# Performance work log

Hardware: AMD Instinct MI355X
Metric: run time of the kernel (lower is better)

Reference implementation:

```python
import jax, jax.numpy as jnp
import numpy as np

NEG = -1e18


def _split_heads(x, h):
    # [B, L, D] -> [B, H, L, D/H]
    b, l, d = x.shape
    return x.reshape(b, l, h, d // h).transpose(0, 2, 1, 3)


def _merge_heads(x):
    # [B, H, L, Dh] -> [B, L, H*Dh]
    b, h, l, dh = x.shape
    return x.transpose(0, 2, 1, 3).reshape(b, l, h * dh)


def _sparse(att, dp_map):
    # att: [B, H, L] per-token scores; dp_map: [B, 2, L] (row, col) tree indices.
    # scatter att[b,h,t] -> S[b, h, dp_map[b,0,t], dp_map[b,1,t]], then symmetrize.
    B, H, L = att.shape
    bi = jnp.arange(B)[:, None, None]          # [B,1,1]
    hi = jnp.arange(H)[None, :, None]          # [1,H,1]
    p0 = dp_map[:, 0, :][:, None, :]           # [B,1,L]
    p1 = dp_map[:, 1, :][:, None, :]           # [B,1,L]
    s = jnp.zeros((B, H, L, L), att.dtype)
    s = s.at[bi, hi, p0, p1].set(att)          # matches torch index_put_ (overwrite)
    return s + jnp.swapaxes(s, 2, 3)


def _reverse(values, dp_map):
    # r[b, j] = values[b, dp_map[b,0,j]] for j >= 1; r[b,0] = 0
    idx = dp_map[:, 0, :]                      # [B, L]
    r = jnp.take_along_axis(values, idx[:, :, None], axis=1)
    return r.at[:, 0, :].set(0.0)


def setup_inputs() -> dict:
    key = jax.random.key(0)
    ks = jax.random.split(key, 16)
    B, L, D, R, H = 16, 384, 768, 768, 12
    inp = {
        "queries":   jax.random.normal(ks[0], (B, L, D), jnp.float32),
        "keys":      jax.random.normal(ks[1], (B, L, D), jnp.float32),
        "values":    jax.random.normal(ks[2], (B, L, D), jnp.float32),
        "relations": jax.random.normal(ks[3], (B, L, R), jnp.float32),
        "dp_map":    jax.random.randint(ks[4], (B, 2, L), 0, L, jnp.int32),
        "mask":      jax.random.bernoulli(ks[5], 0.1, (B, L, L)),
        "rel_mask":  jax.random.bernoulli(ks[6], 0.1, (B, L, 1)),
        "Wq":  jax.random.normal(ks[7],  (D, D), jnp.float32) * 0.02,
        "Wk":  jax.random.normal(ks[8],  (D, D), jnp.float32) * 0.02,
        "Wv":  jax.random.normal(ks[9],  (D, D), jnp.float32) * 0.02,
        "Wo":  jax.random.normal(ks[10], (D, D), jnp.float32) * 0.02,
        "Wge": jax.random.normal(ks[11], (D, R), jnp.float32) * 0.02,
        "Wgr": jax.random.normal(ks[12], (R, R), jnp.float32) * 0.02,
        "Vr":  jax.random.normal(ks[13], (R, 1), jnp.float32) * 0.02,
        "Vg":  jax.random.normal(ks[14], (R, 1), jnp.float32) * 0.02,
    }
    return inp


def reference(queries, keys, values, relations, dp_map, mask, rel_mask,
              Wq, Wk, Wv, Wo, Wge, Wgr, Vr, Vg):
    H = 12
    R = Vg.shape[0]
    Dk = Wq.shape[1]
    scale = (Dk // H) ** -0.5

    # config.is_reverse = True path
    hv = jnp.where(rel_mask, 0.0, _reverse(values, dp_map))       # [B,L,D]
    rel = jnp.where(rel_mask, 0.0, relations)                     # [B,L,R]

    # semantic gated mechanism
    rv_h = _split_heads(rel @ Wgr, H)                             # [B,H,L,R/H]
    hs_h = _split_heads(hv @ Wge, H)
    Vg_h = Vg.reshape(H, R // H, 1)
    g = jnp.tanh(jnp.einsum('bhld,hdo->bhlo', hs_h + rv_h, Vg_h))[..., 0]
    gated = _sparse(g, dp_map)                                    # [B,H,L,L]

    q = _split_heads(queries @ Wq, H) * scale
    k = _split_heads(keys @ Wk, H)
    v = _split_heads(values @ Wv, H)
    rel_h = _split_heads(rel, H)
    Vr_h = Vr.reshape(H, R // H, 1)

    self_logits = jnp.einsum('bhqd,bhkd->bhqk', q, k)             # [B,H,L,L]
    rel_logits = _sparse(jnp.einsum('bhld,hdo->bhlo', rel_h, Vr_h)[..., 0], dp_map)

    m = mask[:, None]                                             # [B,1,L,L]
    self_logits = jnp.where(m, NEG, self_logits)
    rel_logits = jnp.where(m, NEG, rel_logits)

    attention_weights = self_logits.sum(axis=1) / H               # [B,L,L]
    sw = jax.nn.softmax(self_logits, axis=-1)
    rw = jax.nn.softmax(rel_logits, axis=-1)
    w = (1.0 - gated) * sw + gated * rw                           # dropout p=0

    ctx = jnp.einsum('bhqk,bhkd->bhqd', w, v)
    out = _merge_heads(ctx) @ Wo
    return out, attention_weights
```

## Files before the change

### kernel.cpp

```cpp
#include <hip/hip_runtime.h>
#include <math.h>

#define Bn 16
#define Lq 384
#define Hn 12
#define Dm 768
#define DH 64
#define QT2 16
#define NEGV (-1e18f)
#define SPAD 402

typedef __attribute__((ext_vector_type(4))) float f32x4;
typedef __attribute__((ext_vector_type(8))) __bf16 bf16x8;
typedef __attribute__((ext_vector_type(4))) __bf16 bf16x4;
typedef unsigned short ushort_t;
typedef unsigned int uint_t;

__device__ __forceinline__ ushort_t f2b(float f) {
  unsigned int u = __float_as_uint(f);
  unsigned int r = (u + 0x7FFFu + ((u >> 16) & 1u)) >> 16;
  return (ushort_t)r;
}
__device__ __forceinline__ bf16x8 cvt8(float4 a, float4 b) {
  bf16x8 r;
  r[0] = (__bf16)a.x; r[1] = (__bf16)a.y; r[2] = (__bf16)a.z; r[3] = (__bf16)a.w;
  r[4] = (__bf16)b.x; r[5] = (__bf16)b.y; r[6] = (__bf16)b.z; r[7] = (__bf16)b.w;
  return r;
}

__global__ __launch_bounds__(256) void k_prep_age(
    const float* __restrict__ Wge, const float* __restrict__ Wgr,
    const float* __restrict__ Vg, float* __restrict__ Age, float* __restrict__ Agr)
{
  int which = blockIdx.x / Hn;
  int h = blockIdx.x % Hn;
  const float* Wsrc = which ? Wgr : Wge;
  float* dst = which ? Agr : Age;
  __shared__ float vg[DH];
  if (threadIdx.x < DH) vg[threadIdx.x] = Vg[h*DH + threadIdx.x];
  __syncthreads();
  for (int d = threadIdx.x; d < Dm; d += 256) {
    const float* wrow = Wsrc + (size_t)d*Dm + h*DH;
    float s = 0.f;
    #pragma unroll 8
    for (int j = 0; j < DH; ++j) s = fmaf(wrow[j], vg[j], s);
    dst[h*Dm + d] = s;
  }
}

__global__ void k_win(const int* __restrict__ dp, int* __restrict__ win) {
  int i = blockIdx.x*256 + threadIdx.x;
  if (i >= Bn*Lq) return;
  int b = i / Lq, l = i % Lq;
  int p0 = dp[(size_t)(b*2+0)*Lq + l];
  int p1 = dp[(size_t)(b*2+1)*Lq + l];
  atomicMax(&win[(size_t)b*Lq*Lq + (size_t)p0*Lq + p1], l);
}

__global__ __launch_bounds__(256) void k_pair(
    const int* __restrict__ win, const int* __restrict__ mask,
    uint_t* __restrict__ wpair)
{
  __shared__ int tB[32][33];
  int b = blockIdx.z;
  int i0 = blockIdx.x*32, j0 = blockIdx.y*32;
  const int* wb = win + (size_t)b*Lq*Lq;
  const int* mb = mask + (size_t)b*Lq*Lq;
  int tx = threadIdx.x & 31, ty = threadIdx.x >> 5;
  #pragma unroll
  for (int rr = 0; rr < 4; ++rr) {
    int r = ty + rr*8;
    tB[r][tx] = wb[(size_t)(j0+r)*Lq + i0 + tx];
  }
  __syncthreads();
  #pragma unroll
  for (int rr = 0; rr < 4; ++rr) {
    int ti = ty + rr*8;
    int i = i0 + ti, j = j0 + tx;
    int l1 = wb[(size_t)i*Lq + j];
    int l2 = tB[tx][ti];
    int mk = mb[(size_t)i*Lq + j];
    wpair[(size_t)b*Lq*Lq + (size_t)i*Lq + j] =
        ((uint_t)(mk != 0) << 31) | ((unsigned)(l1 + 1) << 16) | (unsigned)(l2 + 1);
  }
}

__global__ __launch_bounds__(256) void k_grlog(
    const float* __restrict__ values, const float* __restrict__ relations,
    const int* __restrict__ dp, const int* __restrict__ rel_mask,
    const float* __restrict__ Age, const float* __restrict__ Agr,
    const float* __restrict__ Vr,
    float* __restrict__ g, float* __restrict__ rlog)
{
  int blk = blockIdx.x;
  int b = blk / (Lq/4), l0 = (blk % (Lq/4))*4;
  int tid = threadIdx.x, lane = tid & 63, wave = tid >> 6;
  __shared__ float relrow[4][Dm], hvrow[4][Dm];
  #pragma unroll
  for (int rr = 0; rr < 4; ++rr) {
    int l = l0 + rr;
    int rm = rel_mask[(size_t)b*Lq + l];
    int idx = dp[(size_t)(b*2)*Lq + l];
    const float* vrow = values + ((size_t)b*Lq + idx)*Dm;
    const float* rrow = relations + ((size_t)b*Lq + l)*Dm;
    for (int d = tid; d < Dm; d += 256) {
      relrow[rr][d] = rm ? 0.f : rrow[d];
      hvrow[rr][d]  = (rm || l == 0) ? 0.f : vrow[d];
    }
  }
  __syncthreads();
  int l = l0 + wave;
  for (int h = 0; h < Hn; ++h) {
    float p = 0.f;
    #pragma unroll
    for (int k = 0; k < Dm/64; ++k) {
      int d = lane + 64*k;
      p = fmaf(hvrow[wave][d], Age[h*Dm + d],
          fmaf(relrow[wave][d], Agr[h*Dm + d], p));
    }
    #pragma unroll
    for (int o = 32; o > 0; o >>= 1) p += __shfl_xor(p, o);
    if (lane == 0) g[((size_t)b*Hn + h)*Lq + l] = tanhf(p);
  }
  if (lane < Hn) {
    float s = 0.f;
    #pragma unroll 8
    for (int j = 0; j < DH; ++j)
      s = fmaf(relrow[wave][lane*DH + j], Vr[lane*DH + j], s);
    rlog[((size_t)b*Hn + lane)*Lq + l] = s;
  }
}

__global__ __launch_bounds__(256) void k_wT4(
    const float* __restrict__ W0, const float* __restrict__ W1,
    const float* __restrict__ W2, const float* __restrict__ W3,
    ushort_t* __restrict__ T0, ushort_t* __restrict__ T1,
    ushort_t* __restrict__ T2, ushort_t* __restrict__ T3)
{
  int z = blockIdx.z;
  const float* W = (z == 0) ? W0 : (z == 1) ? W1 : (z == 2) ? W2 : W3;
  ushort_t* WT = (z == 0) ? T0 : (z == 1) ? T1 : (z == 2) ? T2 : T3;
  __shared__ float t[32][33];
  int k0 = blockIdx.x*32, n0 = blockIdx.y*32;
  int tx = threadIdx.x & 31, ty = threadIdx.x >> 5;
  #pragma unroll
  for (int r = 0; r < 4; ++r)
    t[ty + r*8][tx] = W[(size_t)(k0 + ty + r*8)*Dm + n0 + tx];
  __syncthreads();
  #pragma unroll
  for (int r = 0; r < 4; ++r)
    WT[(size_t)(n0 + ty + r*8)*Dm + k0 + tx] = f2b(t[tx][ty + r*8]);
}

__global__ __launch_bounds__(256) void k_mmqkv(
    const float* __restrict__ Xq, const float* __restrict__ Xk,
    const float* __restrict__ Xv,
    const ushort_t* __restrict__ WqT, const ushort_t* __restrict__ WkT,
    const ushort_t* __restrict__ WvT,
    ushort_t* __restrict__ qbf, ushort_t* __restrict__ kbf,
    ushort_t* __restrict__ vTbf)
{
  const int K = Dm;
  __shared__ ushort_t As[128*64];
  __shared__ ushort_t Bs[128*64];

  int z = blockIdx.z;
  const float* A     = (z == 0) ? Xq : (z == 1) ? Xk : Xv;
  const ushort_t* BT = (z == 0) ? WqT : (z == 1) ? WkT : WvT;

  int bm = blockIdx.x;
  int bn = blockIdx.y;
  int m_blk = bm*128;

  int t = threadIdx.x;
  int wave = t >> 6, lane = t & 63;
  int wr = wave >> 1, wc = wave & 1;
  int lrow = lane & 15, lkg = lane >> 4;

  f32x4 acc[4][4];
  #pragma unroll
  for (int i = 0; i < 4; ++i)
    #pragma unroll
    for (int j = 0; j < 4; ++j) acc[i][j] = (f32x4)(0.f);

  int sr = t >> 3, sc8 = t & 7;
  for (int k0 = 0; k0 < K; k0 += 64) {
    __syncthreads();
    #pragma unroll
    for (int i = 0; i < 4; ++i) {
      int row = sr + i*32;
      const float* ap = A + (size_t)(m_blk + row)*K + k0 + sc8*8;
      float4 f0 = *(const float4*)ap;
      float4 f1 = *(const float4*)(ap + 4);
      uint4 vb = *(const uint4*)(BT + (size_t)(bn*128 + row)*K + k0 + sc8*8);
      int slot = sc8 ^ (row & 7);
      *(bf16x8*)&As[row*64 + slot*8] = cvt8(f0, f1);
      *(uint4*)&Bs[row*64 + slot*8] = vb;
    }
    __syncthreads();
    #pragma unroll
    for (int kk = 0; kk < 2; ++kk) {
      bf16x8 aF[4], bF[4];
      int chunk = kk*4 + lkg;
      #pragma unroll
      for (int mi = 0; mi < 4; ++mi) {
        int arow = wr*64 + mi*16 + lrow;
        aF[mi] = *(const bf16x8*)&As[arow*64 + ((chunk ^ (arow & 7)) << 3)];
        int brow = wc*64 + mi*16 + lrow;
        bF[mi] = *(const bf16x8*)&Bs[brow*64 + ((chunk ^ (brow & 7)) << 3)];
      }
      #pragma unroll
      for (int mi = 0; mi < 4; ++mi)
        #pragma unroll
        for (int ni = 0; ni < 4; ++ni)
          acc[mi][ni] = __builtin_amdgcn_mfma_f32_16x16x32_bf16(
              aF[mi], bF[ni], acc[mi][ni], 0, 0, 0);
    }
  }

  float alpha = (z == 0) ? 0.125f : 1.f;
  #pragma unroll
  for (int mi = 0; mi < 4; ++mi) {
    #pragma unroll
    for (int ni = 0; ni < 4; ++ni) {
      f32x4 a = acc[mi][ni];
      int rit = wr*64 + mi*16 + 4*lkg;
      int cit = wc*64 + ni*16 + lrow;
      int gcol = bn*128 + cit;
      if (z < 2) {
        ushort_t* Cb = z ? kbf : qbf;
        int grow = m_blk + rit;
        #pragma unroll
        for (int r = 0; r < 4; ++r)
          Cb[(size_t)(grow + r)*Dm + gcol] = f2b(a[r]*alpha);
      } else {
        int b = bm/3;
        int rl = (bm%3)*128 + rit;
        ushort4 u;
        u.x = f2b(a[0]); u.y = f2b(a[1]); u.z = f2b(a[2]); u.w = f2b(a[3]);
        *(ushort4*)&vTbf[((size_t)b*Dm + gcol)*Lq + rl] = u;
      }
    }
  }
}

template<int MODE>
__global__ __launch_bounds__(256) void k_mm64(
    const ushort_t* __restrict__ A, const ushort_t* __restrict__ BT,
    float* __restrict__ Cf, const int* __restrict__ mask, float alpha)
{
  const int K = Dm;
  __shared__ ushort_t As[64*64];
  __shared__ ushort_t Bs[128*64];

  int bm = blockIdx.x, bn = blockIdx.y, b = blockIdx.z;
  const ushort_t* Ab = (MODE == 3) ? A  + (size_t)b*Lq*Dm : A;
  const ushort_t* Bb = (MODE == 3) ? BT + (size_t)b*Lq*Dm : BT;
  int m0 = bm*64, n0 = bn*128;

  int t = threadIdx.x;
  int wave = t >> 6, lane = t & 63;
  int wr = wave >> 1, wc = wave & 1;
  int lrow = lane & 15, lkg = lane >> 4;

  f32x4 acc[2][4];
  #pragma unroll
  for (int i = 0; i < 2; ++i)
    #pragma unroll
    for (int j = 0; j < 4; ++j) acc[i][j] = (f32x4)(0.f);

  int sr = t >> 3, sc8 = t & 7;
  for (int k0 = 0; k0 < K; k0 += 64) {
    __syncthreads();
    #pragma unroll
    for (int i = 0; i < 2; ++i) {
      int row = sr + i*32;
      uint4 va = *(const uint4*)(Ab + (size_t)(m0 + row)*K + k0 + sc8*8);
      int slot = sc8 ^ (row & 7);
      *(uint4*)&As[row*64 + slot*8] = va;
    }
    #pragma unroll
    for (int i = 0; i < 4; ++i) {
      int row = sr + i*32;
      uint4 vb = *(const uint4*)(Bb + (size_t)(n0 + row)*K + k0 + sc8*8);
      int slot = sc8 ^ (row & 7);
      *(uint4*)&Bs[row*64 + slot*8] = vb;
    }
    __syncthreads();
    #pragma unroll
    for (int kk = 0; kk < 2; ++kk) {
      bf16x8 aF[2], bF[4];
      int chunk = kk*4 + lkg;
      #pragma unroll
      for (int mi = 0; mi < 2; ++mi) {
        int arow = wr*32 + mi*16 + lrow;
        aF[mi] = *(const bf16x8*)&As[arow*64 + ((chunk ^ (arow & 7)) << 3)];
      }
      #pragma unroll
      for (int ni = 0; ni < 4; ++ni) {
        int brow = wc*64 + ni*16 + lrow;
        bF[ni] = *(const bf16x8*)&Bs[brow*64 + ((chunk ^ (brow & 7)) << 3)];
      }
      #pragma unroll
      for (int mi = 0; mi < 2; ++mi)
        #pragma unroll
        for (int ni = 0; ni < 4; ++ni)
          acc[mi][ni] = __builtin_amdgcn_mfma_f32_16x16x32_bf16(
              aF[mi], bF[ni], acc[mi][ni], 0, 0, 0);
    }
  }

  #pragma unroll
  for (int mi = 0; mi < 2; ++mi) {
    #pragma unroll
    for (int ni = 0; ni < 4; ++ni) {
      f32x4 a = acc[mi][ni];
      int rit = wr*32 + mi*16 + 4*lkg;
      int cit = wc*64 + ni*16 + lrow;
      if (MODE == 0) {
        int grow = m0 + rit, gcol = n0 + cit;
        #pragma unroll
        for (int r = 0; r < 4; ++r)
          Cf[(size_t)(grow + r)*Dm + gcol] = a[r]*alpha;
      } else {
        int rl = m0 + rit, cl = n0 + cit;
        const int* mb2 = mask + (size_t)b*Lq*Lq;
        float* awb = Cf + (size_t)b*Lq*Lq;
        #pragma unroll
        for (int r = 0; r < 4; ++r) {
          int m = mb2[(size_t)(rl + r)*Lq + cl];
          awb[(size_t)(rl + r)*Lq + cl] = m ? NEGV : a[r]*alpha;
        }
      }
    }
  }
}

__global__ __launch_bounds__(256, 5) void k_attn3(
    const ushort_t* __restrict__ qbf, const ushort_t* __restrict__ kbf,
    const ushort_t* __restrict__ vT, const uint_t* __restrict__ wpair,
    const float* __restrict__ g, const float* __restrict__ rlog,
    ushort_t* __restrict__ ctxbf)
{
  __shared__ float S[QT2][SPAD];
  __shared__ float2 rg2[Lq + 1];

  int bid = blockIdx.x;
  int h  = bid % Hn;
  int qt = (bid / Hn) % (Lq/QT2);
  int b  = bid / (Hn * (Lq/QT2));
  int q0 = qt * QT2;
  int tid = threadIdx.x, lane = tid & 63, wave = tid >> 6;
  int lrow = lane & 15, lkg = lane >> 4;
  int w4 = wave*4;

  const uint_t* wpb = wpair + (size_t)b*Lq*Lq;
  const float* gh = g    + ((size_t)b*Hn + h)*Lq;
  const float* rh = rlog + ((size_t)b*Hn + h)*Lq;

  uint_t wpre[4][6];
  #pragma unroll
  for (int r = 0; r < 4; ++r) {
    const uint_t* wrow = wpb + (size_t)(q0 + w4 + r)*Lq + lane;
    #pragma unroll
    for (int u = 0; u < 6; ++u) wpre[r][u] = wrow[u*64];
  }

  if (tid == 0) { rg2[0].x = 0.f; rg2[0].y = 0.f; }
  for (int e = tid; e < Lq; e += 256) {
    float2 v2; v2.x = rh[e]; v2.y = gh[e];
    rg2[e + 1] = v2;
  }

  {
    const ushort_t* qb = qbf + ((size_t)b*Lq + q0 + lrow)*Dm + h*DH + lkg*8;
    bf16x8 aF0 = *(const bf16x8*)(qb);
    bf16x8 aF1 = *(const bf16x8*)(qb + 32);
    int col0 = wave*96;
    f32x4 acc[6];
    #pragma unroll
    for (int tt = 0; tt < 6; ++tt) {
      int col = col0 + tt*16 + lrow;
      const ushort_t* kb = kbf + ((size_t)b*Lq + col)*Dm + h*DH + lkg*8;
      bf16x8 bF0 = *(const bf16x8*)(kb);
      bf16x8 bF1 = *(const bf16x8*)(kb + 32);
      f32x4 z = (f32x4)(0.f);
      z = __builtin_amdgcn_mfma_f32_16x16x32_bf16(aF0, bF0, z, 0, 0, 0);
      z = __builtin_amdgcn_mfma_f32_16x16x32_bf16(aF1, bF1, z, 0, 0, 0);
      acc[tt] = z;
    }
    #pragma unroll
    for (int tt = 0; tt < 6; ++tt) {
      int col = col0 + tt*16 + lrow;
      #pragma unroll
      for (int r = 0; r < 4; ++r)
        S[4*lkg + r][col] = acc[tt][r];
    }
  }
  __syncthreads();

  for (int r = 0; r < 4; ++r) {
    int row = w4 + r;
    float sv[6], rv[6], gv[6];
    #pragma unroll
    for (int u = 0; u < 6; ++u) {
      int kj = u*64 + lane;
      uint_t w = wpre[r][u];
      uint_t i1 = (w >> 16) & 0x7FFFu;
      uint_t i2 = w & 0xFFFFu;
      float2 a = rg2[i1];
      float2 c = rg2[i2];
      bool msk = (int)w < 0;
      sv[u] = msk ? NEGV : S[row][kj];
      rv[u] = msk ? NEGV : (a.x + c.x);
      gv[u] = a.y + c.y;
    }
    float ssum = 0.f, rsum = 0.f;
    #pragma unroll
    for (int u = 0; u < 6; ++u) {
      sv[u] = __expf(sv[u]); ssum += sv[u];
      rv[u] = __expf(rv[u]); rsum += rv[u];
    }
    #pragma unroll
    for (int o = 32; o > 0; o >>= 1) {
      ssum += __shfl_xor(ssum, o);
      rsum += __shfl_xor(rsum, o);
    }
    float si = 1.f/ssum, ri = 1.f/rsum;
    ushort_t* prow = (ushort_t*)&S[row][0];
    #pragma unroll
    for (int u = 0; u < 6; ++u) {
      int kj = u*64 + lane;
      float t1 = sv[u]*si;
      float p = fmaf(gv[u], fmaf(rv[u], ri, -t1), t1);
      prow[kj] = f2b(p);
    }
  }
  __syncthreads();

  {
    int dcol = h*DH + wave*16 + lrow;
    const ushort_t* vb = vT + ((size_t)b*Dm + dcol)*Lq + lkg*8;
    const ushort_t* prow = (const ushort_t*)&S[lrow][0];
    f32x4 o = (f32x4)(0.f);
    #pragma unroll
    for (int ks = 0; ks < 12; ++ks) {
      bf16x4 lo = *(const bf16x4*)(prow + ks*32 + lkg*8);
      bf16x4 hi = *(const bf16x4*)(prow + ks*32 + lkg*8 + 4);
      bf16x8 pa = __builtin_shufflevector(lo, hi, 0,1,2,3,4,5,6,7);
      bf16x8 bv = *(const bf16x8*)(vb + ks*32);
      o = __builtin_amdgcn_mfma_f32_16x16x32_bf16(pa, bv, o, 0, 0, 0);
    }
    #pragma unroll
    for (int r = 0; r < 4; ++r)
      ctxbf[((size_t)b*Lq + q0 + 4*lkg + r)*Dm + dcol] = f2b(o[r]);
  }
}

extern "C" void kernel_launch(void* const* d_in, const int* in_sizes, int n_in,
                              void* d_out, int out_size, void* d_ws, size_t ws_size,
                              hipStream_t stream) {
  const float* queries   = (const float*)d_in[0];
  const float* keys      = (const float*)d_in[1];
  const float* values    = (const float*)d_in[2];
  const float* relations = (const float*)d_in[3];
  const int*   dp_map    = (const int*)d_in[4];
  const int*   mask      = (const int*)d_in[5];
  const int*   rel_mask  = (const int*)d_in[6];
  const float* Wq  = (const float*)d_in[7];
  const float* Wk  = (const float*)d_in[8];
  const float* Wv  = (const float*)d_in[9];
  const float* Wo  = (const float*)d_in[10];
  const float* Wge = (const float*)d_in[11];
  const float* Wgr = (const float*)d_in[12];
  const float* Vr  = (const float*)d_in[13];
  const float* Vg  = (const float*)d_in[14];

  float* ws = (float*)d_ws;
  const size_t SZ   = (size_t)Bn*Lq*Dm;
  const size_t WINS = (size_t)Bn*Lq*Lq;
  const size_t GSZ  = (size_t)Bn*Hn*Lq;

  int*   win  = (int*)ws;
  float* g    = ws + WINS;
  float* rlog = g + GSZ;
  float* Age  = rlog + GSZ;
  float* Agr  = Age + (size_t)Hn*Dm;
  uint_t* wpair = (uint_t*)(Agr + (size_t)Hn*Dm);
  ushort_t* p0 = (ushort_t*)(wpair + WINS);
  ushort_t* qbf  = p0;
  ushort_t* kbf  = p0 + SZ;
  ushort_t* vTbf = p0 + 2*SZ;
  ushort_t* ctxbf= p0 + 3*SZ;
  ushort_t* WqT  = p0 + 4*SZ;
  ushort_t* WkT  = WqT + (size_t)Dm*Dm;
  ushort_t* WvT  = WkT + (size_t)Dm*Dm;
  ushort_t* WoT  = WvT + (size_t)Dm*Dm;

  float* outp = (float*)d_out;
  float* awp  = outp + SZ;

  hipMemsetAsync(win, 0xFF, WINS*sizeof(int), stream);
  k_prep_age<<<2*Hn, 256, 0, stream>>>(Wge, Wgr, Vg, Age, Agr);
  k_win<<<(Bn*Lq + 255)/256, 256, 0, stream>>>(dp_map, win);
  k_grlog<<<Bn*Lq/4, 256, 0, stream>>>(values, relations, dp_map, rel_mask,
                                       Age, Agr, Vr, g, rlog);
  k_wT4<<<dim3(Dm/32, Dm/32, 4), 256, 0, stream>>>(Wq, Wk, Wv, Wo,
                                                   WqT, WkT, WvT, WoT);
  k_mmqkv<<<dim3(48, 6, 3), 256, 0, stream>>>(queries, keys, values,
                                              WqT, WkT, WvT, qbf, kbf, vTbf);
  k_pair<<<dim3(Lq/32, Lq/32, Bn), 256, 0, stream>>>(win, mask, wpair);
  k_mm64<3><<<dim3(6, 3, Bn), 256, 0, stream>>>(qbf, kbf, awp, mask, 1.f/12.f);
  k_attn3<<<Bn*(Lq/QT2)*Hn, 256, 0, stream>>>(qbf, kbf, vTbf, wpair, g, rlog,
                                              ctxbf);
  k_mm64<0><<<dim3(96, 6, 1), 256, 0, stream>>>(ctxbf, WoT, outp, nullptr, 1.f);
}
```

Baseline: 202.7 us.

## Merge prep kernels into one launch and store exp scores as bf16 in LDS

Three small preprocessing kernels (Age/Agr reduction, weight transpose, and the dp_map winner atomics) are merged into one launch with block-range dispatch, removing two kernel launches. In the attention kernel, self-attention scores are exponentiated right after the MFMA and stored as bf16 in shared memory instead of fp32. This halves the LDS footprint, and launch bounds are raised to allow more resident blocks. The trade-off is that there is no max-subtraction, and exp values are rounded to bf16 before summing, which lowers precision and risks overflow for large logits.

```diff
diff --git a/kernel.cpp b/kernel.cpp
--- a/kernel.cpp
+++ b/kernel.cpp
@@ -8,7 +8,7 @@
 #define DH 64
 #define QT2 16
 #define NEGV (-1e18f)
-#define SPAD 402
+#define SPADU 404
 
 typedef __attribute__((ext_vector_type(4))) float f32x4;
 typedef __attribute__((ext_vector_type(8))) __bf16 bf16x8;
@@ -21,6 +21,9 @@
   unsigned int r = (u + 0x7FFFu + ((u >> 16) & 1u)) >> 16;
   return (ushort_t)r;
 }
+__device__ __forceinline__ float b2f(ushort_t u) {
+  return __uint_as_float(((unsigned int)u) << 16);
+}
 __device__ __forceinline__ bf16x8 cvt8(float4 a, float4 b) {
   bf16x8 r;
   r[0] = (__bf16)a.x; r[1] = (__bf16)a.y; r[2] = (__bf16)a.z; r[3] = (__bf16)a.w;
@@ -28,33 +31,54 @@
   return r;
 }
 
-__global__ __launch_bounds__(256) void k_prep_age(
+__global__ __launch_bounds__(256) void k_prep(
     const float* __restrict__ Wge, const float* __restrict__ Wgr,
-    const float* __restrict__ Vg, float* __restrict__ Age, float* __restrict__ Agr)
+    const float* __restrict__ Vg,
+    float* __restrict__ Age, float* __restrict__ Agr,
+    const float* __restrict__ W0, const float* __restrict__ W1,
+    const float* __restrict__ W2, const float* __restrict__ W3,
+    ushort_t* __restrict__ T0, ushort_t* __restrict__ T1,
+    ushort_t* __restrict__ T2, ushort_t* __restrict__ T3,
+    const int* __restrict__ dp, int* __restrict__ win)
 {
-  int which = blockIdx.x / Hn;
-  int h = blockIdx.x % Hn;
-  const float* Wsrc = which ? Wgr : Wge;
-  float* dst = which ? Agr : Age;
   __shared__ float vg[DH];
-  if (threadIdx.x < DH) vg[threadIdx.x] = Vg[h*DH + threadIdx.x];
-  __syncthreads();
-  for (int d = threadIdx.x; d < Dm; d += 256) {
-    const float* wrow = Wsrc + (size_t)d*Dm + h*DH;
-    float s = 0.f;
-    #pragma unroll 8
-    for (int j = 0; j < DH; ++j) s = fmaf(wrow[j], vg[j], s);
-    dst[h*Dm + d] = s;
-  }
-}
-
-__global__ void k_win(const int* __restrict__ dp, int* __restrict__ win) {
-  int i = blockIdx.x*256 + threadIdx.x;
-  if (i >= Bn*Lq) return;
-  int b = i / Lq, l = i % Lq;
-  int p0 = dp[(size_t)(b*2+0)*Lq + l];
-  int p1 = dp[(size_t)(b*2+1)*Lq + l];
-  atomicMax(&win[(size_t)b*Lq*Lq + (size_t)p0*Lq + p1], l);
+  __shared__ float t[32][33];
+  int blk = blockIdx.x;
+  if (blk < 24) {
+    int which = blk / Hn;
+    int h = blk % Hn;
+    const float* Wsrc = which ? Wgr : Wge;
+    float* dst = which ? Agr : Age;
+    if (threadIdx.x < DH) vg[threadIdx.x] = Vg[h*DH + threadIdx.x];
+    __syncthreads();
+    for (int d = threadIdx.x; d < Dm; d += 256) {
+      const float* wrow = Wsrc + (size_t)d*Dm + h*DH;
+      float s = 0.f;
+      #pragma unroll 8
+      for (int j = 0; j < DH; ++j) s = fmaf(wrow[j], vg[j], s);
+      dst[h*Dm + d] = s;
+    }
+  } else if (blk < 24 + 2304) {
+    int b2 = blk - 24;
+    int z = b2 / 576, rem = b2 % 576;
+    const float* W = (z == 0) ? W0 : (z == 1) ? W1 : (z == 2) ? W2 : W3;
+    ushort_t* WT = (z == 0) ? T0 : (z == 1) ? T1 : (z == 2) ? T2 : T3;
+    int k0 = (rem / 24)*32, n0 = (rem % 24)*32;
+    int tx = threadIdx.x & 31, ty = threadIdx.x >> 5;
+    #pragma unroll
+    for (int r = 0; r < 4; ++r)
+      t[ty + r*8][tx] = W[(size_t)(k0 + ty + r*8)*Dm + n0 + tx];
+    __syncthreads();
+    #pragma unroll
+    for (int r = 0; r < 4; ++r)
+      WT[(size_t)(n0 + ty + r*8)*Dm + k0 + tx] = f2b(t[tx][ty + r*8]);
+  } else {
+    int i = (blk - 2328)*256 + threadIdx.x;
+    int b = i / Lq, l = i % Lq;
+    int p0 = dp[(size_t)(b*2+0)*Lq + l];
+    int p1 = dp[(size_t)(b*2+1)*Lq + l];
+    atomicMax(&win[(size_t)b*Lq*Lq + (size_t)p0*Lq + p1], l);
+  }
 }
 
 __global__ __launch_bounds__(256) void k_pair(
@@ -129,27 +153,6 @@
       s = fmaf(relrow[wave][lane*DH + j], Vr[lane*DH + j], s);
     rlog[((size_t)b*Hn + lane)*Lq + l] = s;
   }
-}
-
-__global__ __launch_bounds__(256) void k_wT4(
-    const float* __restrict__ W0, const float* __restrict__ W1,
-    const float* __restrict__ W2, const float* __restrict__ W3,
-    ushort_t* __restrict__ T0, ushort_t* __restrict__ T1,
-    ushort_t* __restrict__ T2, ushort_t* __restrict__ T3)
-{
-  int z = blockIdx.z;
-  const float* W = (z == 0) ? W0 : (z == 1) ? W1 : (z == 2) ? W2 : W3;
-  ushort_t* WT = (z == 0) ? T0 : (z == 1) ? T1 : (z == 2) ? T2 : T3;
-  __shared__ float t[32][33];
-  int k0 = blockIdx.x*32, n0 = blockIdx.y*32;
-  int tx = threadIdx.x & 31, ty = threadIdx.x >> 5;
-  #pragma unroll
-  for (int r = 0; r < 4; ++r)
-    t[ty + r*8][tx] = W[(size_t)(k0 + ty + r*8)*Dm + n0 + tx];
-  __syncthreads();
-  #pragma unroll
-  for (int r = 0; r < 4; ++r)
-    WT[(size_t)(n0 + ty + r*8)*Dm + k0 + tx] = f2b(t[tx][ty + r*8]);
 }
 
 __global__ __launch_bounds__(256) void k_mmqkv(
@@ -336,13 +339,13 @@
   }
 }
 
-__global__ __launch_bounds__(256, 5) void k_attn3(
+__global__ __launch_bounds__(256, 8) void k_attn3(
     const ushort_t* __restrict__ qbf, const ushort_t* __restrict__ kbf,
     const ushort_t* __restrict__ vT, const uint_t* __restrict__ wpair,
     const float* __restrict__ g, const float* __restrict__ rlog,
     ushort_t* __restrict__ ctxbf)
 {
-  __shared__ float S[QT2][SPAD];
+  __shared__ ushort_t S16[QT2][SPADU];
   __shared__ float2 rg2[Lq + 1];
 
   int bid = blockIdx.x;
@@ -377,7 +380,6 @@
     bf16x8 aF0 = *(const bf16x8*)(qb);
     bf16x8 aF1 = *(const bf16x8*)(qb + 32);
     int col0 = wave*96;
-    f32x4 acc[6];
     #pragma unroll
     for (int tt = 0; tt < 6; ++tt) {
       int col = col0 + tt*16 + lrow;
@@ -387,14 +389,9 @@
       f32x4 z = (f32x4)(0.f);
       z = __builtin_amdgcn_mfma_f32_16x16x32_bf16(aF0, bF0, z, 0, 0, 0);
       z = __builtin_amdgcn_mfma_f32_16x16x32_bf16(aF1, bF1, z, 0, 0, 0);
-      acc[tt] = z;
-    }
-    #pragma unroll
-    for (int tt = 0; tt < 6; ++tt) {
-      int col = col0 + tt*16 + lrow;
       #pragma unroll
       for (int r = 0; r < 4; ++r)
-        S[4*lkg + r][col] = acc[tt][r];
+        S16[4*lkg + r][col] = f2b(__expf(z[r]));
     }
   }
   __syncthreads();
@@ -402,6 +399,7 @@
   for (int r = 0; r < 4; ++r) {
     int row = w4 + r;
     float sv[6], rv[6], gv[6];
+    float ssum = 0.f, rsum = 0.f;
     #pragma unroll
     for (int u = 0; u < 6; ++u) {
       int kj = u*64 + lane;
@@ -411,15 +409,10 @@
       float2 a = rg2[i1];
       float2 c = rg2[i2];
       bool msk = (int)w < 0;
-      sv[u] = msk ? NEGV : S[row][kj];
-      rv[u] = msk ? NEGV : (a.x + c.x);
+      sv[u] = msk ? 0.f : b2f(S16[row][kj]);
+      rv[u] = msk ? 0.f : __expf(a.x + c.x);
       gv[u] = a.y + c.y;
-    }
-    float ssum = 0.f, rsum = 0.f;
-    #pragma unroll
-    for (int u = 0; u < 6; ++u) {
-      sv[u] = __expf(sv[u]); ssum += sv[u];
-      rv[u] = __expf(rv[u]); rsum += rv[u];
+      ssum += sv[u]; rsum += rv[u];
     }
     #pragma unroll
     for (int o = 32; o > 0; o >>= 1) {
@@ -427,7 +420,7 @@
       rsum += __shfl_xor(rsum, o);
     }
     float si = 1.f/ssum, ri = 1.f/rsum;
-    ushort_t* prow = (ushort_t*)&S[row][0];
+    ushort_t* prow = &S16[row][0];
     #pragma unroll
     for (int u = 0; u < 6; ++u) {
       int kj = u*64 + lane;
@@ -441,7 +434,7 @@
   {
     int dcol = h*DH + wave*16 + lrow;
     const ushort_t* vb = vT + ((size_t)b*Dm + dcol)*Lq + lkg*8;
-    const ushort_t* prow = (const ushort_t*)&S[lrow][0];
+    const ushort_t* prow = &S16[lrow][0];
     f32x4 o = (f32x4)(0.f);
     #pragma unroll
     for (int ks = 0; ks < 12; ++ks) {
@@ -501,12 +494,11 @@
   float* awp  = outp + SZ;
 
   hipMemsetAsync(win, 0xFF, WINS*sizeof(int), stream);
-  k_prep_age<<<2*Hn, 256, 0, stream>>>(Wge, Wgr, Vg, Age, Agr);
-  k_win<<<(Bn*Lq + 255)/256, 256, 0, stream>>>(dp_map, win);
+  k_prep<<<2352, 256, 0, stream>>>(Wge, Wgr, Vg, Age, Agr,
+                                   Wq, Wk, Wv, Wo, WqT, WkT, WvT, WoT,
+                                   dp_map, win);
   k_grlog<<<Bn*Lq/4, 256, 0, stream>>>(values, relations, dp_map, rel_mask,
                                        Age, Agr, Vr, g, rlog);
-  k_wT4<<<dim3(Dm/32, Dm/32, 4), 256, 0, stream>>>(Wq, Wk, Wv, Wo,
-                                                   WqT, WkT, WvT, WoT);
   k_mmqkv<<<dim3(48, 6, 3), 256, 0, stream>>>(queries, keys, values,
                                               WqT, WkT, WvT, qbf, kbf, vTbf);
   k_pair<<<dim3(Lq/32, Lq/32, Bn), 256, 0, stream>>>(win, mask, wpair);
```

Result: faster. 197.3 us (-2.7%).
